# Kernel tuning notes

Hardware: AMD Instinct MI355X
Metric: run time of the kernel (lower is better)

The kernel has to match this reference:

```python
import jax, jax.numpy as jnp
import numpy as np

N = 100000   # nodes
E = 1600000  # edges
D = 64       # in_channel == out_channel
NEG_SLOPE = 0.01  # nn.LeakyReLU default


def gcn_conv(x, W, b, src, dst, n):
    # PyG GCNConv: add self-loops, sym-normalize by in-degree (at col/dst),
    # norm(e) = deg[src]^-1/2 * deg[dst]^-1/2, aggregate at dst, then + bias.
    deg = jnp.zeros((n,), x.dtype).at[dst].add(1.0) + 1.0  # in-degree incl. self-loop
    dinv = jax.lax.rsqrt(deg)
    h = x @ W                                   # [N, Dout]
    coef = (dinv[src] * dinv[dst])[:, None]     # [E, 1]
    agg = jax.ops.segment_sum(h[src] * coef, dst, num_segments=n)  # scatter-add
    # self-loop contribution: deg[i]^-1 * h[i]
    return agg + (dinv * dinv)[:, None] * h + b


def setup_inputs() -> dict:
    key = jax.random.key(0)
    ks = jax.random.split(key, 10)
    x = jax.random.normal(ks[0], (N, D), dtype=jnp.float32)
    edge_index = jax.random.randint(ks[1], (2, E), 0, N)
    s = 1.0 / np.sqrt(D)  # glorot-ish scale
    inp = {"x": x, "edge_index": edge_index}
    for i in range(4):
        inp[f"W{i+1}"] = jax.random.normal(ks[2 + i], (D, D), dtype=jnp.float32) * s
        inp[f"b{i+1}"] = jnp.zeros((D,), dtype=jnp.float32)
    return inp


def reference(x, edge_index, W1, b1, W2, b2, W3, b3, W4, b4):
    # eval mode: F.dropout(training=False) is identity, so omitted.
    src, dst = edge_index[0], edge_index[1]
    h = x
    for W, b in ((W1, b1), (W2, b2), (W3, b3), (W4, b4)):
        h = gcn_conv(h, W, b, src, dst, N)
        h = jnp.where(h >= 0, h, NEG_SLOPE * h)  # LeakyReLU
    return h
```

## Files before the change

kernel.cpp:

```cpp
#include <hip/hip_runtime.h>
#include <hip/hip_fp16.h>

#define N_NODES 100000
#define N_EDGES 1600000
#define DIM 64
#define NEG_SLOPE 0.01f

#define BNODES 128
#define NBUCK 782
#define BCAP 4096
#define BLOCKS1 256
#define THREADS1 1024
#define EPB (N_EDGES / BLOCKS1)

typedef _Float16 half8 __attribute__((ext_vector_type(8)));
typedef float float4v __attribute__((ext_vector_type(4)));

__global__ void prep_weights(const float* __restrict__ W0, const float* __restrict__ W1,
                             const float* __restrict__ W2, const float* __restrict__ W3,
                             __half* __restrict__ WT16) {
    const float* Ws[4] = {W0, W1, W2, W3};
    const float* W = Ws[blockIdx.x];
    __half* dst = WT16 + (size_t)blockIdx.x * DIM * DIM;
    for (int e = threadIdx.x; e < DIM * DIM; e += 256) {
        int k = e >> 6, f = e & 63;
        dst[f * DIM + k] = __float2half(W[e]);
    }
}

__global__ __launch_bounds__(THREADS1) void bucket_scatter(const int* __restrict__ src,
                                                           const int* __restrict__ dst,
                                                           int* __restrict__ gcur,
                                                           int* __restrict__ bdata) {
    __shared__ int cnt[NBUCK];
    __shared__ int cur[NBUCK];
    __shared__ int lexcl[NBUCK];
    __shared__ int base[NBUCK];
    __shared__ int scan[THREADS1];
    __shared__ int sorted_e[EPB];
    __shared__ unsigned short sorted_b[EPB];

    const int tid = threadIdx.x;
    for (int i = tid; i < NBUCK; i += THREADS1) { cnt[i] = 0; cur[i] = 0; }
    __syncthreads();

    const int e0 = blockIdx.x * EPB;
    const int e1 = e0 + EPB;

    for (int e = e0 + tid; e < e1; e += THREADS1)
        atomicAdd(&cnt[dst[e] >> 7], 1);
    __syncthreads();

    int v = (tid < NBUCK) ? cnt[tid] : 0;
    scan[tid] = v;
    __syncthreads();
    for (int s = 1; s < THREADS1; s <<= 1) {
        int a = (tid >= s) ? scan[tid - s] : 0;
        __syncthreads();
        scan[tid] += a;
        __syncthreads();
    }
    if (tid < NBUCK) lexcl[tid] = scan[tid] - v;

    if (tid < NBUCK) {
        int c = cnt[tid];
        base[tid] = c ? atomicAdd(&gcur[tid * 16], c) : 0;
    }
    __syncthreads();

    for (int e = e0 + tid; e < e1; e += THREADS1) {
        int d = dst[e];
        int b = d >> 7;
        int p = lexcl[b] + atomicAdd(&cur[b], 1);
        sorted_e[p] = src[e] | ((d & 127) << 17);
        sorted_b[p] = (unsigned short)b;
    }
    __syncthreads();

    for (int i = tid; i < EPB; i += THREADS1) {
        int b = sorted_b[i];
        bdata[(size_t)b * BCAP + base[b] + (i - lexcl[b])] = sorted_e[i];
    }
}

__global__ __launch_bounds__(256) void bucket_build(const int* __restrict__ bdata,
                                                    const int* __restrict__ gcur,
                                                    int* __restrict__ offsets,
                                                    float* __restrict__ dinv,
                                                    int* __restrict__ csr) {
    __shared__ int cnt[BNODES];
    __shared__ int excl[BNODES];
    __shared__ int part[256];
    const int tid = threadIdx.x;
    const int b = blockIdx.x;
    const int sz = gcur[b * 16];
    const int* bd = bdata + (size_t)b * BCAP;

    int s = 0;
    for (int i = tid; i < b; i += 256) s += gcur[i * 16];
    part[tid] = s;
    __syncthreads();
    for (int st = 128; st > 0; st >>= 1) {
        if (tid < st) part[tid] += part[tid + st];
        __syncthreads();
    }
    const int cbase = part[0];
    __syncthreads();

    for (int i = tid; i < BNODES; i += 256) cnt[i] = 0;
    __syncthreads();
    for (int i = tid; i < sz; i += 256)
        atomicAdd(&cnt[bd[i] >> 17], 1);
    __syncthreads();
    if (tid == 0) {
        int run = 0;
        for (int j = 0; j < BNODES; ++j) { excl[j] = run; run += cnt[j]; }
    }
    __syncthreads();

    const int nb = b * BNODES;
    for (int i = tid; i < BNODES; i += 256) {
        int n = nb + i;
        if (n < N_NODES) {
            offsets[n] = cbase + excl[i];
            dinv[n] = rsqrtf((float)(cnt[i] + 1));
        }
    }
    if (b == NBUCK - 1 && tid == 0) offsets[N_NODES] = N_EDGES;

    for (int i = tid; i < BNODES; i += 256) cnt[i] = 0;
    __syncthreads();
    for (int i = tid; i < sz; i += 256) {
        int v = bd[i];
        int l = v >> 17;
        int pos = cbase + excl[l] + atomicAdd(&cnt[l], 1);
        csr[pos] = (v & 0x1FFFF) << 6;
    }
}

__device__ __forceinline__ void stage8(__half* dst, const float* __restrict__ X, size_t off) {
    float4 f0 = *(const float4*)(X + off);
    float4 f1 = *(const float4*)(X + off + 4);
    __half2 h0 = __floats2half2_rn(f0.x, f0.y);
    __half2 h1 = __floats2half2_rn(f0.z, f0.w);
    __half2 h2 = __floats2half2_rn(f1.x, f1.y);
    __half2 h3 = __floats2half2_rn(f1.z, f1.w);
    uint4 u;
    u.x = *(unsigned int*)&h0; u.y = *(unsigned int*)&h1;
    u.z = *(unsigned int*)&h2; u.w = *(unsigned int*)&h3;
    *(uint4*)dst = u;
}
__device__ __forceinline__ void stage8(__half* dst, const __half* __restrict__ X, size_t off) {
    *(uint4*)dst = *(const uint4*)(X + off);
}

#define XPAD 72
template <typename TIN>
__global__ __launch_bounds__(256) void mm_kernel(const TIN* __restrict__ X,
                                                 const __half* __restrict__ WT,
                                                 const float* __restrict__ dinv,
                                                 __half* __restrict__ G16) {
    __shared__ __align__(16) __half xs[64][XPAD];
    __shared__ __align__(16) __half ws[64][XPAD];
    const int t = threadIdx.x;
    const int rbase = blockIdx.x * 64;

    for (int c = t; c < 512; c += 256) {
        int row = c >> 3, koff = (c & 7) * 8;
        int grow = rbase + row;
        if (grow < N_NODES) {
            stage8(&xs[row][koff], X, (size_t)grow * DIM + koff);
        } else {
            *(uint4*)&xs[row][koff] = make_uint4(0, 0, 0, 0);
        }
        stage8(&ws[row][koff], WT, (size_t)row * DIM + koff);
    }
    __syncthreads();

    const int wave = t >> 6;
    const int lane = t & 63;
    const int q = lane >> 4;
    const int c16 = lane & 15;
    const int n0 = wave * 16;

    half8 b0 = *(const half8*)&xs[n0 + c16][q * 8];
    half8 b1 = *(const half8*)&xs[n0 + c16][32 + q * 8];

    const int gnode = rbase + n0 + c16;
    float di = (gnode < N_NODES) ? dinv[gnode] : 0.f;

#pragma unroll
    for (int ft = 0; ft < 4; ++ft) {
        const int f0 = ft * 16;
        half8 a0 = *(const half8*)&ws[f0 + c16][q * 8];
        half8 a1 = *(const half8*)&ws[f0 + c16][32 + q * 8];
        float4v acc = {0.f, 0.f, 0.f, 0.f};
        acc = __builtin_amdgcn_mfma_f32_16x16x32_f16(a0, b0, acc, 0, 0, 0);
        acc = __builtin_amdgcn_mfma_f32_16x16x32_f16(a1, b1, acc, 0, 0, 0);
        if (gnode < N_NODES) {
            __half2 p0 = __floats2half2_rn(di * acc[0], di * acc[1]);
            __half2 p1 = __floats2half2_rn(di * acc[2], di * acc[3]);
            uint2 u;
            u.x = *(unsigned int*)&p0;
            u.y = *(unsigned int*)&p1;
            *(uint2*)(G16 + (size_t)gnode * DIM + f0 + q * 4) = u;
        }
    }
}

#define AGG_BLOCKS 2048
#define AGG_WAVES (AGG_BLOCKS * 4)
#define NPAIRS (N_NODES / 2)
template <bool FINAL>
__global__ __launch_bounds__(256) void agg_kernel(const __half* __restrict__ G16,
                                                  const int* __restrict__ csr,
                                                  const int* __restrict__ offsets,
                                                  const float* __restrict__ dinv,
                                                  const float* __restrict__ bias,
                                                  void* __restrict__ outp) {
    const int gw = (blockIdx.x * 256 + threadIdx.x) >> 6;
    const int lane = threadIdx.x & 63;
    const int grp  = lane >> 5;
    const int slot = (lane >> 3) & 3;
    const int sub  = lane & 7;
    const int fc   = sub * 8;

    for (int p = gw; p < NPAIRS; p += AGG_WAVES) {
        const int wid = p * 2 + grp;
        const int beg = offsets[wid], end = offsets[wid + 1];

        __half2 h0 = __float2half2_rn(0.f), h1 = h0, h2 = h0, h3 = h0;

#define PKACC(vraw)                                     \
        {                                               \
            const __half2* hp = (const __half2*)&(vraw);\
            h0 = __hadd2(h0, hp[0]);                    \
            h1 = __hadd2(h1, hp[1]);                    \
            h2 = __hadd2(h2, hp[2]);                    \
            h3 = __hadd2(h3, hp[3]);                    \
        }

        int e = beg + slot;
        for (; e + 4 < end; e += 8) {
            int p0 = csr[e];
            int p1 = csr[e + 4];
            float4 v0 = *(const float4*)(G16 + (size_t)p0 + fc);
            float4 v1 = *(const float4*)(G16 + (size_t)p1 + fc);
            PKACC(v0)
            PKACC(v1)
        }
        if (e < end) {
            int p0 = csr[e];
            float4 v0 = *(const float4*)(G16 + (size_t)p0 + fc);
            PKACC(v0)
        }
#undef PKACC

        float acc[8];
        {
            float2 f;
            f = __half22float2(h0); acc[0] = f.x; acc[1] = f.y;
            f = __half22float2(h1); acc[2] = f.x; acc[3] = f.y;
            f = __half22float2(h2); acc[4] = f.x; acc[5] = f.y;
            f = __half22float2(h3); acc[6] = f.x; acc[7] = f.y;
        }
#pragma unroll
        for (int k = 0; k < 8; ++k) {
            acc[k] += __shfl_xor(acc[k], 8, 64);
            acc[k] += __shfl_xor(acc[k], 16, 64);
        }

        if (slot == 0) {
            float4 vs = *(const float4*)(G16 + (size_t)wid * DIM + fc);
            {
                const __half2* hp = (const __half2*)&vs;
                float2 f0 = __half22float2(hp[0]);
                float2 f1 = __half22float2(hp[1]);
                float2 f2 = __half22float2(hp[2]);
                float2 f3 = __half22float2(hp[3]);
                acc[0] += f0.x; acc[1] += f0.y;
                acc[2] += f1.x; acc[3] += f1.y;
                acc[4] += f2.x; acc[5] += f2.y;
                acc[6] += f3.x; acc[7] += f3.y;
            }

            float di = dinv[wid];
            float4 b0 = *(const float4*)(bias + fc);
            float4 b1 = *(const float4*)(bias + fc + 4);
            float r[8];
            r[0] = di * acc[0] + b0.x;
            r[1] = di * acc[1] + b0.y;
            r[2] = di * acc[2] + b0.z;
            r[3] = di * acc[3] + b0.w;
            r[4] = di * acc[4] + b1.x;
            r[5] = di * acc[5] + b1.y;
            r[6] = di * acc[6] + b1.z;
            r[7] = di * acc[7] + b1.w;
#pragma unroll
            for (int k = 0; k < 8; ++k)
                r[k] = (r[k] >= 0.f) ? r[k] : NEG_SLOPE * r[k];

            if (FINAL) {
                float* out = (float*)outp;
                *(float4*)(out + (size_t)wid * DIM + fc)     = make_float4(r[0], r[1], r[2], r[3]);
                *(float4*)(out + (size_t)wid * DIM + fc + 4) = make_float4(r[4], r[5], r[6], r[7]);
            } else {
                __half* act = (__half*)outp;
                __half2 q0 = __floats2half2_rn(r[0], r[1]);
                __half2 q1 = __floats2half2_rn(r[2], r[3]);
                __half2 q2 = __floats2half2_rn(r[4], r[5]);
                __half2 q3 = __floats2half2_rn(r[6], r[7]);
                uint4 u;
                u.x = *(unsigned int*)&q0;
                u.y = *(unsigned int*)&q1;
                u.z = *(unsigned int*)&q2;
                u.w = *(unsigned int*)&q3;
                *(uint4*)(act + (size_t)wid * DIM + fc) = u;
            }
        }
    }
}

extern "C" void kernel_launch(void* const* d_in, const int* in_sizes, int n_in,
                              void* d_out, int out_size, void* d_ws, size_t ws_size,
                              hipStream_t stream) {
    const float* x = (const float*)d_in[0];
    const int* ei = (const int*)d_in[1];
    const int* src = ei;
    const int* dst = ei + N_EDGES;
    const float* W[4] = {(const float*)d_in[2], (const float*)d_in[4],
                         (const float*)d_in[6], (const float*)d_in[8]};
    const float* b[4] = {(const float*)d_in[3], (const float*)d_in[5],
                         (const float*)d_in[7], (const float*)d_in[9]};
    float* out = (float*)d_out;

    char* ws = (char*)d_ws;
    size_t off = 0;
    auto alloc = [&](size_t bytes) -> void* {
        void* p = ws + off;
        off = (off + bytes + 255) & ~(size_t)255;
        return p;
    };
    __half* G16   = (__half*)alloc((size_t)N_NODES * DIM * sizeof(__half));
    __half* ACT16 = (__half*)alloc((size_t)N_NODES * DIM * sizeof(__half));
    __half* WT16  = (__half*)alloc((size_t)4 * DIM * DIM * sizeof(__half));
    int*   csr    = (int*)alloc((size_t)N_EDGES * sizeof(int));
    int*   bdata  = (int*)alloc((size_t)NBUCK * BCAP * sizeof(int));
    int*   gcur   = (int*)alloc((size_t)NBUCK * 16 * sizeof(int));
    int*   offsets= (int*)alloc((size_t)(N_NODES + 1) * sizeof(int));
    float* dinv   = (float*)alloc((size_t)N_NODES * sizeof(float));

    hipMemsetAsync(gcur, 0, (size_t)NBUCK * 16 * sizeof(int), stream);
    prep_weights<<<4, 256, 0, stream>>>(W[0], W[1], W[2], W[3], WT16);

    bucket_scatter<<<BLOCKS1, THREADS1, 0, stream>>>(src, dst, gcur, bdata);
    bucket_build<<<NBUCK, 256, 0, stream>>>(bdata, gcur, offsets, dinv, csr);

    const int MM_GRID = (N_NODES + 63) / 64;

    mm_kernel<float><<<MM_GRID, 256, 0, stream>>>(x, WT16, dinv, G16);
    agg_kernel<false><<<AGG_BLOCKS, 256, 0, stream>>>(G16, csr, offsets, dinv, b[0], ACT16);
    mm_kernel<__half><<<MM_GRID, 256, 0, stream>>>(ACT16, WT16 + DIM * DIM, dinv, G16);
    agg_kernel<false><<<AGG_BLOCKS, 256, 0, stream>>>(G16, csr, offsets, dinv, b[1], ACT16);
    mm_kernel<__half><<<MM_GRID, 256, 0, stream>>>(ACT16, WT16 + 2 * DIM * DIM, dinv, G16);
    agg_kernel<false><<<AGG_BLOCKS, 256, 0, stream>>>(G16, csr, offsets, dinv, b[2], ACT16);
    mm_kernel<__half><<<MM_GRID, 256, 0, stream>>>(ACT16, WT16 + 3 * DIM * DIM, dinv, G16);
    agg_kernel<true><<<AGG_BLOCKS, 256, 0, stream>>>(G16, csr, offsets, dinv, b[3], out);
}
```

Measured before the change: 310.4 us.

## Fuse aggregation with the next layer's matmul and shrink node buckets to 64

Adds a fused_agg_mm kernel that, per block of 64 nodes, gathers and sums neighbor features, applies normalization, bias and LeakyReLU, keeps the activations in shared memory, and immediately multiplies them by the next layer's weights with MFMA. Layers 1-3 use it, which removes the separate mm launch and the round-trip of the intermediate activation buffer through global memory. Bucket granularity drops from 128 to 64 nodes so one block maps to one bucket, which changes the scatter-scan to handle two buckets per thread. The cost is a coarser grid, with each wave walking 8 nodes serially, and that may reduce latency hiding in the gather-bound phase.

```diff
diff --git a/kernel.cpp b/kernel.cpp
--- a/kernel.cpp
+++ b/kernel.cpp
@@ -6,9 +6,9 @@
 #define DIM 64
 #define NEG_SLOPE 0.01f
 
-#define BNODES 128
-#define NBUCK 782
-#define BCAP 4096
+#define BNODES 64
+#define NBUCK 1563
+#define BCAP 2048
 #define BLOCKS1 256
 #define THREADS1 1024
 #define EPB (N_EDGES / BLOCKS1)
@@ -48,10 +48,15 @@
     const int e1 = e0 + EPB;
 
     for (int e = e0 + tid; e < e1; e += THREADS1)
-        atomicAdd(&cnt[dst[e] >> 7], 1);
-    __syncthreads();
-
-    int v = (tid < NBUCK) ? cnt[tid] : 0;
+        atomicAdd(&cnt[dst[e] >> 6], 1);
+    __syncthreads();
+
+    int v = 0;
+    const int HALF = (NBUCK + 1) / 2;
+    if (tid < HALF) {
+        v = cnt[2 * tid];
+        if (2 * tid + 1 < NBUCK) v += cnt[2 * tid + 1];
+    }
     scan[tid] = v;
     __syncthreads();
     for (int s = 1; s < THREADS1; s <<= 1) {
@@ -60,19 +65,23 @@
         scan[tid] += a;
         __syncthreads();
     }
-    if (tid < NBUCK) lexcl[tid] = scan[tid] - v;
-
-    if (tid < NBUCK) {
-        int c = cnt[tid];
-        base[tid] = c ? atomicAdd(&gcur[tid * 16], c) : 0;
+    if (tid < HALF) {
+        int ex = scan[tid] - v;
+        lexcl[2 * tid] = ex;
+        if (2 * tid + 1 < NBUCK) lexcl[2 * tid + 1] = ex + cnt[2 * tid];
+    }
+
+    for (int i = tid; i < NBUCK; i += THREADS1) {
+        int c = cnt[i];
+        base[i] = c ? atomicAdd(&gcur[i * 16], c) : 0;
     }
     __syncthreads();
 
     for (int e = e0 + tid; e < e1; e += THREADS1) {
         int d = dst[e];
-        int b = d >> 7;
+        int b = d >> 6;
         int p = lexcl[b] + atomicAdd(&cur[b], 1);
-        sorted_e[p] = src[e] | ((d & 127) << 17);
+        sorted_e[p] = src[e] | ((d & 63) << 17);
         sorted_b[p] = (unsigned short)b;
     }
     __syncthreads();
@@ -204,6 +213,151 @@
             u.x = *(unsigned int*)&p0;
             u.y = *(unsigned int*)&p1;
             *(uint2*)(G16 + (size_t)gnode * DIM + f0 + q * 4) = u;
+        }
+    }
+}
+
+__global__ __launch_bounds__(256) void fused_agg_mm(const __half* __restrict__ Gin,
+                                                    const int* __restrict__ csr,
+                                                    const int* __restrict__ offsets,
+                                                    const float* __restrict__ dinv,
+                                                    const float* __restrict__ bias,
+                                                    const __half* __restrict__ WT,
+                                                    __half* __restrict__ Gout) {
+    __shared__ __align__(16) __half act[64][XPAD];
+    __shared__ __align__(16) __half ws[64][XPAD];
+    const int t = threadIdx.x;
+    const int blk = blockIdx.x;
+    const int nb = blk * BNODES;
+
+    for (int c = t; c < 512; c += 256) {
+        int row = c >> 3, koff = (c & 7) * 8;
+        stage8(&ws[row][koff], WT, (size_t)row * DIM + koff);
+    }
+
+    const int wave = t >> 6;
+    const int lane = t & 63;
+    const int grp  = lane >> 5;
+    const int slot = (lane >> 3) & 3;
+    const int sub  = lane & 7;
+    const int fc   = sub * 8;
+
+    for (int i = 0; i < 8; ++i) {
+        const int lrow = wave * 16 + i * 2 + grp;
+        const int wid = nb + lrow;
+        const bool valid = (wid < N_NODES);
+        const int beg = valid ? offsets[wid] : 0;
+        const int end = valid ? offsets[wid + 1] : 0;
+
+        __half2 h0 = __float2half2_rn(0.f), h1 = h0, h2 = h0, h3 = h0;
+
+#define PKACC(vraw)                                     \
+        {                                               \
+            const __half2* hp = (const __half2*)&(vraw);\
+            h0 = __hadd2(h0, hp[0]);                    \
+            h1 = __hadd2(h1, hp[1]);                    \
+            h2 = __hadd2(h2, hp[2]);                    \
+            h3 = __hadd2(h3, hp[3]);                    \
+        }
+        int e = beg + slot;
+        for (; e + 4 < end; e += 8) {
+            int p0 = csr[e];
+            int p1 = csr[e + 4];
+            float4 v0 = *(const float4*)(Gin + (size_t)p0 + fc);
+            float4 v1 = *(const float4*)(Gin + (size_t)p1 + fc);
+            PKACC(v0)
+            PKACC(v1)
+        }
+        if (e < end) {
+            int p0 = csr[e];
+            float4 v0 = *(const float4*)(Gin + (size_t)p0 + fc);
+            PKACC(v0)
+        }
+#undef PKACC
+
+        float acc[8];
+        {
+            float2 f;
+            f = __half22float2(h0); acc[0] = f.x; acc[1] = f.y;
+            f = __half22float2(h1); acc[2] = f.x; acc[3] = f.y;
+            f = __half22float2(h2); acc[4] = f.x; acc[5] = f.y;
+            f = __half22float2(h3); acc[6] = f.x; acc[7] = f.y;
+        }
+#pragma unroll
+        for (int k = 0; k < 8; ++k) {
+            acc[k] += __shfl_xor(acc[k], 8, 64);
+            acc[k] += __shfl_xor(acc[k], 16, 64);
+        }
+
+        if (slot == 0) {
+            uint4 u = make_uint4(0, 0, 0, 0);
+            if (valid) {
+                float4 vs = *(const float4*)(Gin + (size_t)wid * DIM + fc);
+                {
+                    const __half2* hp = (const __half2*)&vs;
+                    float2 f0 = __half22float2(hp[0]);
+                    float2 f1 = __half22float2(hp[1]);
+                    float2 f2 = __half22float2(hp[2]);
+                    float2 f3 = __half22float2(hp[3]);
+                    acc[0] += f0.x; acc[1] += f0.y;
+                    acc[2] += f1.x; acc[3] += f1.y;
+                    acc[4] += f2.x; acc[5] += f2.y;
+                    acc[6] += f3.x; acc[7] += f3.y;
+                }
+                float di = dinv[wid];
+                float4 bb0 = *(const float4*)(bias + fc);
+                float4 bb1 = *(const float4*)(bias + fc + 4);
+                float r[8];
+                r[0] = di * acc[0] + bb0.x;
+                r[1] = di * acc[1] + bb0.y;
+                r[2] = di * acc[2] + bb0.z;
+                r[3] = di * acc[3] + bb0.w;
+                r[4] = di * acc[4] + bb1.x;
+                r[5] = di * acc[5] + bb1.y;
+                r[6] = di * acc[6] + bb1.z;
+                r[7] = di * acc[7] + bb1.w;
+#pragma unroll
+                for (int k = 0; k < 8; ++k)
+                    r[k] = (r[k] >= 0.f) ? r[k] : NEG_SLOPE * r[k];
+                __half2 q0 = __floats2half2_rn(r[0], r[1]);
+                __half2 q1 = __floats2half2_rn(r[2], r[3]);
+                __half2 q2 = __floats2half2_rn(r[4], r[5]);
+                __half2 q3 = __floats2half2_rn(r[6], r[7]);
+                u.x = *(unsigned int*)&q0;
+                u.y = *(unsigned int*)&q1;
+                u.z = *(unsigned int*)&q2;
+                u.w = *(unsigned int*)&q3;
+            }
+            *(uint4*)(&act[lrow][fc]) = u;
+        }
+    }
+    __syncthreads();
+
+    const int q = lane >> 4;
+    const int c16 = lane & 15;
+    const int n0 = wave * 16;
+
+    half8 xb0 = *(const half8*)&act[n0 + c16][q * 8];
+    half8 xb1 = *(const half8*)&act[n0 + c16][32 + q * 8];
+
+    const int gnode = nb + n0 + c16;
+    float dio = (gnode < N_NODES) ? dinv[gnode] : 0.f;
+
+#pragma unroll
+    for (int ft = 0; ft < 4; ++ft) {
+        const int f0 = ft * 16;
+        half8 a0 = *(const half8*)&ws[f0 + c16][q * 8];
+        half8 a1 = *(const half8*)&ws[f0 + c16][32 + q * 8];
+        float4v accv = {0.f, 0.f, 0.f, 0.f};
+        accv = __builtin_amdgcn_mfma_f32_16x16x32_f16(a0, xb0, accv, 0, 0, 0);
+        accv = __builtin_amdgcn_mfma_f32_16x16x32_f16(a1, xb1, accv, 0, 0, 0);
+        if (gnode < N_NODES) {
+            __half2 p0 = __floats2half2_rn(dio * accv[0], dio * accv[1]);
+            __half2 p1 = __floats2half2_rn(dio * accv[2], dio * accv[3]);
+            uint2 u;
+            u.x = *(unsigned int*)&p0;
+            u.y = *(unsigned int*)&p1;
+            *(uint2*)(Gout + (size_t)gnode * DIM + f0 + q * 4) = u;
         }
     }
 }
@@ -341,8 +495,8 @@
         off = (off + bytes + 255) & ~(size_t)255;
         return p;
     };
-    __half* G16   = (__half*)alloc((size_t)N_NODES * DIM * sizeof(__half));
-    __half* ACT16 = (__half*)alloc((size_t)N_NODES * DIM * sizeof(__half));
+    __half* GA    = (__half*)alloc((size_t)N_NODES * DIM * sizeof(__half));
+    __half* GB    = (__half*)alloc((size_t)N_NODES * DIM * sizeof(__half));
     __half* WT16  = (__half*)alloc((size_t)4 * DIM * DIM * sizeof(__half));
     int*   csr    = (int*)alloc((size_t)N_EDGES * sizeof(int));
     int*   bdata  = (int*)alloc((size_t)NBUCK * BCAP * sizeof(int));
@@ -358,12 +512,9 @@
 
     const int MM_GRID = (N_NODES + 63) / 64;
 
-    mm_kernel<float><<<MM_GRID, 256, 0, stream>>>(x, WT16, dinv, G16);
-    agg_kernel<false><<<AGG_BLOCKS, 256, 0, stream>>>(G16, csr, offsets, dinv, b[0], ACT16);
-    mm_kernel<__half><<<MM_GRID, 256, 0, stream>>>(ACT16, WT16 + DIM * DIM, dinv, G16);
-    agg_kernel<false><<<AGG_BLOCKS, 256, 0, stream>>>(G16, csr, offsets, dinv, b[1], ACT16);
-    mm_kernel<__half><<<MM_GRID, 256, 0, stream>>>(ACT16, WT16 + 2 * DIM * DIM, dinv, G16);
-    agg_kernel<false><<<AGG_BLOCKS, 256, 0, stream>>>(G16, csr, offsets, dinv, b[2], ACT16);
-    mm_kernel<__half><<<MM_GRID, 256, 0, stream>>>(ACT16, WT16 + 3 * DIM * DIM, dinv, G16);
-    agg_kernel<true><<<AGG_BLOCKS, 256, 0, stream>>>(G16, csr, offsets, dinv, b[3], out);
-}
+    mm_kernel<float><<<MM_GRID, 256, 0, stream>>>(x, WT16, dinv, GA);
+    fused_agg_mm<<<NBUCK, 256, 0, stream>>>(GA, csr, offsets, dinv, b[0], WT16 + 1 * DIM * DIM, GB);
+    fused_agg_mm<<<NBUCK, 256, 0, stream>>>(GB, csr, offsets, dinv, b[1], WT16 + 2 * DIM * DIM, GA);
+    fused_agg_mm<<<NBUCK, 256, 0, stream>>>(GA, csr, offsets, dinv, b[2], WT16 + 3 * DIM * DIM, GB);
+    agg_kernel<true><<<AGG_BLOCKS, 256, 0, stream>>>(GB, csr, offsets, dinv, b[3], out);
+}
```

New measurement: 292.4 us. 5.8% less time.

## Split features into quarter planes for cache-resident aggregation and coarsen CSR buckets

Applied to the files above, without the earlier changes.

Intermediate features are stored in four feature-quarter planes of 16 halves per node, so each aggregation block gathers from one 3.2MB plane that can stay cache-resident, instead of from the whole 12.8MB row-major array. The aggregation grid is now 4x1563 blocks over fixed 64-node ranges, with 16 edge slots per node, 2 lanes per slot and a wider shuffle reduction. The CSR build moves to 256-node buckets with 512-thread scatter blocks and a wave-shuffle scan, and the gcur memset is folded into prep_weights. The cost is four passes over the CSR and offsets per layer, and each gather is only 32 bytes wide.

```diff
diff --git a/kernel.cpp b/kernel.cpp
--- a/kernel.cpp
+++ b/kernel.cpp
@@ -6,25 +6,35 @@
 #define DIM 64
 #define NEG_SLOPE 0.01f
 
-#define BNODES 128
-#define NBUCK 782
-#define BCAP 4096
-#define BLOCKS1 256
-#define THREADS1 1024
+#define PNODES 256
+#define PNB 391
+#define BCAP 4608
+#define BLOCKS1 512
+#define THREADS1 512
 #define EPB (N_EDGES / BLOCKS1)
+
+#define FNODES 64
+#define FNB 1563
+#define QELEM 16
+#define QSTRIDE ((size_t)N_NODES * QELEM)
 
 typedef _Float16 half8 __attribute__((ext_vector_type(8)));
 typedef float float4v __attribute__((ext_vector_type(4)));
 
 __global__ void prep_weights(const float* __restrict__ W0, const float* __restrict__ W1,
                              const float* __restrict__ W2, const float* __restrict__ W3,
-                             __half* __restrict__ WT16) {
-    const float* Ws[4] = {W0, W1, W2, W3};
-    const float* W = Ws[blockIdx.x];
-    __half* dst = WT16 + (size_t)blockIdx.x * DIM * DIM;
-    for (int e = threadIdx.x; e < DIM * DIM; e += 256) {
-        int k = e >> 6, f = e & 63;
-        dst[f * DIM + k] = __float2half(W[e]);
+                             __half* __restrict__ WT16, int* __restrict__ gcur) {
+    if (blockIdx.x < 4) {
+        const float* Ws[4] = {W0, W1, W2, W3};
+        const float* W = Ws[blockIdx.x];
+        __half* dst = WT16 + (size_t)blockIdx.x * DIM * DIM;
+        for (int e = threadIdx.x; e < DIM * DIM; e += 256) {
+            int k = e >> 6, f = e & 63;
+            dst[f * DIM + k] = __float2half(W[e]);
+        }
+    } else {
+        for (int i = (blockIdx.x - 4) * 256 + threadIdx.x; i < PNB * 16; i += 4 * 256)
+            gcur[i] = 0;
     }
 }
 
@@ -32,47 +42,49 @@
                                                            const int* __restrict__ dst,
                                                            int* __restrict__ gcur,
                                                            int* __restrict__ bdata) {
-    __shared__ int cnt[NBUCK];
-    __shared__ int cur[NBUCK];
-    __shared__ int lexcl[NBUCK];
-    __shared__ int base[NBUCK];
-    __shared__ int scan[THREADS1];
+    __shared__ int cnt[PNB];
+    __shared__ int lexcl[PNB];
+    __shared__ int base[PNB];
+    __shared__ int wsum[THREADS1 / 64];
     __shared__ int sorted_e[EPB];
     __shared__ unsigned short sorted_b[EPB];
 
     const int tid = threadIdx.x;
-    for (int i = tid; i < NBUCK; i += THREADS1) { cnt[i] = 0; cur[i] = 0; }
+    for (int i = tid; i < PNB; i += THREADS1) cnt[i] = 0;
     __syncthreads();
 
     const int e0 = blockIdx.x * EPB;
     const int e1 = e0 + EPB;
 
     for (int e = e0 + tid; e < e1; e += THREADS1)
-        atomicAdd(&cnt[dst[e] >> 7], 1);
-    __syncthreads();
-
-    int v = (tid < NBUCK) ? cnt[tid] : 0;
-    scan[tid] = v;
-    __syncthreads();
-    for (int s = 1; s < THREADS1; s <<= 1) {
-        int a = (tid >= s) ? scan[tid - s] : 0;
-        __syncthreads();
-        scan[tid] += a;
-        __syncthreads();
-    }
-    if (tid < NBUCK) lexcl[tid] = scan[tid] - v;
-
-    if (tid < NBUCK) {
-        int c = cnt[tid];
-        base[tid] = c ? atomicAdd(&gcur[tid * 16], c) : 0;
+        atomicAdd(&cnt[dst[e] >> 8], 1);
+    __syncthreads();
+
+    int v = (tid < PNB) ? cnt[tid] : 0;
+    int incl = v;
+#pragma unroll
+    for (int s = 1; s < 64; s <<= 1) {
+        int up = __shfl_up(incl, s, 64);
+        if ((tid & 63) >= s) incl += up;
+    }
+    if ((tid & 63) == 63) wsum[tid >> 6] = incl;
+    __syncthreads();
+    int wpre = 0;
+    for (int w = 0; w < (tid >> 6); ++w) wpre += wsum[w];
+    if (tid < PNB) lexcl[tid] = wpre + incl - v;
+
+    for (int i = tid; i < PNB; i += THREADS1) {
+        int c = cnt[i];
+        base[i] = c ? atomicAdd(&gcur[i * 16], c) : 0;
+        cnt[i] = 0;
     }
     __syncthreads();
 
     for (int e = e0 + tid; e < e1; e += THREADS1) {
         int d = dst[e];
-        int b = d >> 7;
-        int p = lexcl[b] + atomicAdd(&cur[b], 1);
-        sorted_e[p] = src[e] | ((d & 127) << 17);
+        int b = d >> 8;
+        int p = lexcl[b] + atomicAdd(&cnt[b], 1);
+        sorted_e[p] = src[e] | ((d & 255) << 17);
         sorted_b[p] = (unsigned short)b;
     }
     __syncthreads();
@@ -88,8 +100,8 @@
                                                     int* __restrict__ offsets,
                                                     float* __restrict__ dinv,
                                                     int* __restrict__ csr) {
-    __shared__ int cnt[BNODES];
-    __shared__ int excl[BNODES];
+    __shared__ int cnt[PNODES];
+    __shared__ int excl[PNODES];
     __shared__ int part[256];
     const int tid = threadIdx.x;
     const int b = blockIdx.x;
@@ -107,38 +119,40 @@
     const int cbase = part[0];
     __syncthreads();
 
-    for (int i = tid; i < BNODES; i += 256) cnt[i] = 0;
+    for (int i = tid; i < PNODES; i += 256) cnt[i] = 0;
     __syncthreads();
     for (int i = tid; i < sz; i += 256)
         atomicAdd(&cnt[bd[i] >> 17], 1);
     __syncthreads();
     if (tid == 0) {
         int run = 0;
-        for (int j = 0; j < BNODES; ++j) { excl[j] = run; run += cnt[j]; }
-    }
-    __syncthreads();
-
-    const int nb = b * BNODES;
-    for (int i = tid; i < BNODES; i += 256) {
+        for (int j = 0; j < PNODES; ++j) { excl[j] = run; run += cnt[j]; }
+    }
+    __syncthreads();
+
+    const int nb = b * PNODES;
+    for (int i = tid; i < PNODES; i += 256) {
         int n = nb + i;
         if (n < N_NODES) {
             offsets[n] = cbase + excl[i];
             dinv[n] = rsqrtf((float)(cnt[i] + 1));
         }
     }
-    if (b == NBUCK - 1 && tid == 0) offsets[N_NODES] = N_EDGES;
-
-    for (int i = tid; i < BNODES; i += 256) cnt[i] = 0;
+    if (b == PNB - 1 && tid == 0) offsets[N_NODES] = N_EDGES;
+
+    for (int i = tid; i < PNODES; i += 256) cnt[i] = 0;
     __syncthreads();
     for (int i = tid; i < sz; i += 256) {
         int v = bd[i];
         int l = v >> 17;
         int pos = cbase + excl[l] + atomicAdd(&cnt[l], 1);
-        csr[pos] = (v & 0x1FFFF) << 6;
-    }
-}
-
-__device__ __forceinline__ void stage8(__half* dst, const float* __restrict__ X, size_t off) {
+        csr[pos] = (v & 0x1FFFF) << 4;
+    }
+}
+
+__device__ __forceinline__ void stage_row8(__half* dst, const float* __restrict__ X,
+                                           int node, int koff) {
+    size_t off = (size_t)node * DIM + koff;
     float4 f0 = *(const float4*)(X + off);
     float4 f1 = *(const float4*)(X + off + 4);
     __half2 h0 = __floats2half2_rn(f0.x, f0.y);
@@ -150,8 +164,10 @@
     u.z = *(unsigned int*)&h2; u.w = *(unsigned int*)&h3;
     *(uint4*)dst = u;
 }
-__device__ __forceinline__ void stage8(__half* dst, const __half* __restrict__ X, size_t off) {
-    *(uint4*)dst = *(const uint4*)(X + off);
+__device__ __forceinline__ void stage_row8(__half* dst, const __half* __restrict__ X,
+                                           int node, int koff) {
+    const __half* p = X + (size_t)(koff >> 4) * QSTRIDE + (size_t)node * QELEM + (koff & 15);
+    *(uint4*)dst = *(const uint4*)p;
 }
 
 #define XPAD 72
@@ -169,22 +185,25 @@
         int row = c >> 3, koff = (c & 7) * 8;
         int grow = rbase + row;
         if (grow < N_NODES) {
-            stage8(&xs[row][koff], X, (size_t)grow * DIM + koff);
+            stage_row8(&xs[row][koff], X, grow, koff);
         } else {
             *(uint4*)&xs[row][koff] = make_uint4(0, 0, 0, 0);
         }
-        stage8(&ws[row][koff], WT, (size_t)row * DIM + koff);
+        {
+            const __half* p = WT + (size_t)row * DIM + koff;
+            *(uint4*)&ws[row][koff] = *(const uint4*)p;
+        }
     }
     __syncthreads();
 
     const int wave = t >> 6;
     const int lane = t & 63;
-    const int q = lane >> 4;
+    const int qr = lane >> 4;
     const int c16 = lane & 15;
     const int n0 = wave * 16;
 
-    half8 b0 = *(const half8*)&xs[n0 + c16][q * 8];
-    half8 b1 = *(const half8*)&xs[n0 + c16][32 + q * 8];
+    half8 b0 = *(const half8*)&xs[n0 + c16][qr * 8];
+    half8 b1 = *(const half8*)&xs[n0 + c16][32 + qr * 8];
 
     const int gnode = rbase + n0 + c16;
     float di = (gnode < N_NODES) ? dinv[gnode] : 0.f;
@@ -192,8 +211,8 @@
 #pragma unroll
     for (int ft = 0; ft < 4; ++ft) {
         const int f0 = ft * 16;
-        half8 a0 = *(const half8*)&ws[f0 + c16][q * 8];
-        half8 a1 = *(const half8*)&ws[f0 + c16][32 + q * 8];
+        half8 a0 = *(const half8*)&ws[f0 + c16][qr * 8];
+        half8 a1 = *(const half8*)&ws[f0 + c16][32 + qr * 8];
         float4v acc = {0.f, 0.f, 0.f, 0.f};
         acc = __builtin_amdgcn_mfma_f32_16x16x32_f16(a0, b0, acc, 0, 0, 0);
         acc = __builtin_amdgcn_mfma_f32_16x16x32_f16(a1, b1, acc, 0, 0, 0);
@@ -203,58 +222,51 @@
             uint2 u;
             u.x = *(unsigned int*)&p0;
             u.y = *(unsigned int*)&p1;
-            *(uint2*)(G16 + (size_t)gnode * DIM + f0 + q * 4) = u;
-        }
-    }
-}
-
-#define AGG_BLOCKS 2048
-#define AGG_WAVES (AGG_BLOCKS * 4)
-#define NPAIRS (N_NODES / 2)
+            __half* gp = G16 + (size_t)(f0 >> 4) * QSTRIDE + (size_t)gnode * QELEM + qr * 4;
+            *(uint2*)gp = u;
+        }
+    }
+}
+
 template <bool FINAL>
-__global__ __launch_bounds__(256) void agg_kernel(const __half* __restrict__ G16,
-                                                  const int* __restrict__ csr,
-                                                  const int* __restrict__ offsets,
-                                                  const float* __restrict__ dinv,
-                                                  const float* __restrict__ bias,
-                                                  void* __restrict__ outp) {
-    const int gw = (blockIdx.x * 256 + threadIdx.x) >> 6;
-    const int lane = threadIdx.x & 63;
+__global__ __launch_bounds__(256) void agg4(const __half* __restrict__ Gin,
+                                            const int* __restrict__ csr,
+                                            const int* __restrict__ offsets,
+                                            const float* __restrict__ dinv,
+                                            const float* __restrict__ bias,
+                                            void* __restrict__ outp) {
+    const int bid = blockIdx.x;
+    const int q = bid / FNB;
+    const int bucket = bid - q * FNB;
+    const int nb = bucket * FNODES;
+    const __half* Gq = Gin + (size_t)q * QSTRIDE;
+
+    const int t = threadIdx.x;
+    const int wave = t >> 6;
+    const int lane = t & 63;
     const int grp  = lane >> 5;
-    const int slot = (lane >> 3) & 3;
-    const int sub  = lane & 7;
-    const int fc   = sub * 8;
-
-    for (int p = gw; p < NPAIRS; p += AGG_WAVES) {
-        const int wid = p * 2 + grp;
-        const int beg = offsets[wid], end = offsets[wid + 1];
+    const int g    = lane & 31;
+    const int slot = g >> 1;
+    const int sub  = g & 1;
+    const int fo   = sub * 8;
+
+    for (int i = 0; i < 8; ++i) {
+        const int lrow = wave * 16 + i * 2 + grp;
+        const int wid = nb + lrow;
+        const bool valid = (wid < N_NODES);
+        const int beg = valid ? offsets[wid] : 0;
+        const int end = valid ? offsets[wid + 1] : 0;
 
         __half2 h0 = __float2half2_rn(0.f), h1 = h0, h2 = h0, h3 = h0;
-
-#define PKACC(vraw)                                     \
-        {                                               \
-            const __half2* hp = (const __half2*)&(vraw);\
-            h0 = __hadd2(h0, hp[0]);                    \
-            h1 = __hadd2(h1, hp[1]);                    \
-            h2 = __hadd2(h2, hp[2]);                    \
-            h3 = __hadd2(h3, hp[3]);                    \
-        }
-
-        int e = beg + slot;
-        for (; e + 4 < end; e += 8) {
+        for (int e = beg + slot; e < end; e += 16) {
             int p0 = csr[e];
-            int p1 = csr[e + 4];
-            float4 v0 = *(const float4*)(G16 + (size_t)p0 + fc);
-            float4 v1 = *(const float4*)(G16 + (size_t)p1 + fc);
-            PKACC(v0)
-            PKACC(v1)
-        }
-        if (e < end) {
-            int p0 = csr[e];
-            float4 v0 = *(const float4*)(G16 + (size_t)p0 + fc);
-            PKACC(v0)
-        }
-#undef PKACC
+            float4 v0 = *(const float4*)(Gq + (size_t)p0 + fo);
+            const __half2* hp = (const __half2*)&v0;
+            h0 = __hadd2(h0, hp[0]);
+            h1 = __hadd2(h1, hp[1]);
+            h2 = __hadd2(h2, hp[2]);
+            h3 = __hadd2(h3, hp[3]);
+        }
 
         float acc[8];
         {
@@ -266,12 +278,14 @@
         }
 #pragma unroll
         for (int k = 0; k < 8; ++k) {
+            acc[k] += __shfl_xor(acc[k], 2, 64);
+            acc[k] += __shfl_xor(acc[k], 4, 64);
             acc[k] += __shfl_xor(acc[k], 8, 64);
             acc[k] += __shfl_xor(acc[k], 16, 64);
         }
 
-        if (slot == 0) {
-            float4 vs = *(const float4*)(G16 + (size_t)wid * DIM + fc);
+        if (slot == 0 && valid) {
+            float4 vs = *(const float4*)(Gq + (size_t)wid * QELEM + fo);
             {
                 const __half2* hp = (const __half2*)&vs;
                 float2 f0 = __half22float2(hp[0]);
@@ -283,27 +297,26 @@
                 acc[4] += f2.x; acc[5] += f2.y;
                 acc[6] += f3.x; acc[7] += f3.y;
             }
-
             float di = dinv[wid];
-            float4 b0 = *(const float4*)(bias + fc);
-            float4 b1 = *(const float4*)(bias + fc + 4);
+            float4 bb0 = *(const float4*)(bias + q * QELEM + fo);
+            float4 bb1 = *(const float4*)(bias + q * QELEM + fo + 4);
             float r[8];
-            r[0] = di * acc[0] + b0.x;
-            r[1] = di * acc[1] + b0.y;
-            r[2] = di * acc[2] + b0.z;
-            r[3] = di * acc[3] + b0.w;
-            r[4] = di * acc[4] + b1.x;
-            r[5] = di * acc[5] + b1.y;
-            r[6] = di * acc[6] + b1.z;
-            r[7] = di * acc[7] + b1.w;
+            r[0] = di * acc[0] + bb0.x;
+            r[1] = di * acc[1] + bb0.y;
+            r[2] = di * acc[2] + bb0.z;
+            r[3] = di * acc[3] + bb0.w;
+            r[4] = di * acc[4] + bb1.x;
+            r[5] = di * acc[5] + bb1.y;
+            r[6] = di * acc[6] + bb1.z;
+            r[7] = di * acc[7] + bb1.w;
 #pragma unroll
             for (int k = 0; k < 8; ++k)
                 r[k] = (r[k] >= 0.f) ? r[k] : NEG_SLOPE * r[k];
 
             if (FINAL) {
                 float* out = (float*)outp;
-                *(float4*)(out + (size_t)wid * DIM + fc)     = make_float4(r[0], r[1], r[2], r[3]);
-                *(float4*)(out + (size_t)wid * DIM + fc + 4) = make_float4(r[4], r[5], r[6], r[7]);
+                *(float4*)(out + (size_t)wid * DIM + q * QELEM + fo)     = make_float4(r[0], r[1], r[2], r[3]);
+                *(float4*)(out + (size_t)wid * DIM + q * QELEM + fo + 4) = make_float4(r[4], r[5], r[6], r[7]);
             } else {
                 __half* act = (__half*)outp;
                 __half2 q0 = __floats2half2_rn(r[0], r[1]);
@@ -315,7 +328,7 @@
                 u.y = *(unsigned int*)&q1;
                 u.z = *(unsigned int*)&q2;
                 u.w = *(unsigned int*)&q3;
-                *(uint4*)(act + (size_t)wid * DIM + fc) = u;
+                *(uint4*)(act + (size_t)q * QSTRIDE + (size_t)wid * QELEM + fo) = u;
             }
         }
     }
@@ -341,29 +354,30 @@
         off = (off + bytes + 255) & ~(size_t)255;
         return p;
     };
-    __half* G16   = (__half*)alloc((size_t)N_NODES * DIM * sizeof(__half));
+    __half* GA    = (__half*)alloc((size_t)N_NODES * DIM * sizeof(__half));
+    __half* GB    = (__half*)alloc((size_t)N_NODES * DIM * sizeof(__half));
     __half* ACT16 = (__half*)alloc((size_t)N_NODES * DIM * sizeof(__half));
     __half* WT16  = (__half*)alloc((size_t)4 * DIM * DIM * sizeof(__half));
     int*   csr    = (int*)alloc((size_t)N_EDGES * sizeof(int));
-    int*   bdata  = (int*)alloc((size_t)NBUCK * BCAP * sizeof(int));
-    int*   gcur   = (int*)alloc((size_t)NBUCK * 16 * sizeof(int));
+    int*   bdata  = (int*)alloc((size_t)PNB * BCAP * sizeof(int));
+    int*   gcur   = (int*)alloc((size_t)PNB * 16 * sizeof(int));
     int*   offsets= (int*)alloc((size_t)(N_NODES + 1) * sizeof(int));
     float* dinv   = (float*)alloc((size_t)N_NODES * sizeof(float));
 
-    hipMemsetAsync(gcur, 0, (size_t)NBUCK * 16 * sizeof(int), stream);
-    prep_weights<<<4, 256, 0, stream>>>(W[0], W[1], W[2], W[3], WT16);
+    prep_weights<<<8, 256, 0, stream>>>(W[0], W[1], W[2], W[3], WT16, gcur);
 
     bucket_scatter<<<BLOCKS1, THREADS1, 0, stream>>>(src, dst, gcur, bdata);
-    bucket_build<<<NBUCK, 256, 0, stream>>>(bdata, gcur, offsets, dinv, csr);
+    bucket_build<<<PNB, 256, 0, stream>>>(bdata, gcur, offsets, dinv, csr);
 
     const int MM_GRID = (N_NODES + 63) / 64;
-
-    mm_kernel<float><<<MM_GRID, 256, 0, stream>>>(x, WT16, dinv, G16);
-    agg_kernel<false><<<AGG_BLOCKS, 256, 0, stream>>>(G16, csr, offsets, dinv, b[0], ACT16);
-    mm_kernel<__half><<<MM_GRID, 256, 0, stream>>>(ACT16, WT16 + DIM * DIM, dinv, G16);
-    agg_kernel<false><<<AGG_BLOCKS, 256, 0, stream>>>(G16, csr, offsets, dinv, b[1], ACT16);
-    mm_kernel<__half><<<MM_GRID, 256, 0, stream>>>(ACT16, WT16 + 2 * DIM * DIM, dinv, G16);
-    agg_kernel<false><<<AGG_BLOCKS, 256, 0, stream>>>(G16, csr, offsets, dinv, b[2], ACT16);
-    mm_kernel<__half><<<MM_GRID, 256, 0, stream>>>(ACT16, WT16 + 3 * DIM * DIM, dinv, G16);
-    agg_kernel<true><<<AGG_BLOCKS, 256, 0, stream>>>(G16, csr, offsets, dinv, b[3], out);
-}
+    const int AGG_GRID = 4 * FNB;
+
+    mm_kernel<float><<<MM_GRID, 256, 0, stream>>>(x, WT16, dinv, GA);
+    agg4<false><<<AGG_GRID, 256, 0, stream>>>(GA, csr, offsets, dinv, b[0], ACT16);
+    mm_kernel<__half><<<MM_GRID, 256, 0, stream>>>(ACT16, WT16 + 1 * DIM * DIM, dinv, GB);
+    agg4<false><<<AGG_GRID, 256, 0, stream>>>(GB, csr, offsets, dinv, b[1], ACT16);
+    mm_kernel<__half><<<MM_GRID, 256, 0, stream>>>(ACT16, WT16 + 2 * DIM * DIM, dinv, GA);
+    agg4<false><<<AGG_GRID, 256, 0, stream>>>(GA, csr, offsets, dinv, b[2], ACT16);
+    mm_kernel<__half><<<MM_GRID, 256, 0, stream>>>(ACT16, WT16 + 3 * DIM * DIM, dinv, GB);
+    agg4<true><<<AGG_GRID, 256, 0, stream>>>(GB, csr, offsets, dinv, b[3], out);
+}
```

After: 493.2 us. 1.59x slower.
